# Optimization experiments

Hardware: AMD Instinct MI355X
Metric: run time of the kernel (lower is better)

Reference implementation:

```python
import jax, jax.numpy as jnp
import numpy as np

C = 256
R = 16
K = 7


def setup_inputs() -> dict:
    key = jax.random.key(0)
    k1, k2, k3, k4 = jax.random.split(key, 4)
    x = jax.random.normal(k1, (32, C, 64, 64), dtype=jnp.float32)
    # mlp: Conv2d(C, C//R, 1, bias=False) then Conv2d(C//R, C, 1, bias=False)
    w1 = jax.random.normal(k2, (C // R, C), dtype=jnp.float32) * (1.0 / np.sqrt(C))
    w2 = jax.random.normal(k3, (C, C // R), dtype=jnp.float32) * (1.0 / np.sqrt(C // R))
    # conv_spatial: Conv2d(2, 1, 7, padding=3, bias=False) -> OIHW [1,2,7,7]
    w_sp = jax.random.normal(k4, (1, 2, K, K), dtype=jnp.float32) * (1.0 / np.sqrt(2 * K * K))
    return {"x": x, "w1": w1, "w2": w2, "w_sp": w_sp}


def _cbam(x, w1, w2, w_sp):
    B, Cc, H, W = x.shape
    # --- channel attention ---
    avg = jnp.mean(x, axis=(2, 3))            # [B, C]
    mx = jnp.max(x, axis=(2, 3))              # [B, C]

    def mlp(v):
        h = jax.nn.relu(jnp.einsum('bc,rc->br', v, w1))  # [B, C//R]
        return jnp.einsum('br,cr->bc', h, w2)            # [B, C]

    ch_att = jax.nn.sigmoid(mlp(avg) + mlp(mx))          # [B, C]
    x = x * ch_att[:, :, None, None]

    # --- spatial attention ---
    avg_sp = jnp.mean(x, axis=1, keepdims=True)          # [B,1,H,W]
    max_sp = jnp.max(x, axis=1, keepdims=True)           # [B,1,H,W]
    sp = jnp.concatenate([avg_sp, max_sp], axis=1)       # [B,2,H,W]
    att = jax.lax.conv_general_dilated(
        sp, w_sp, window_strides=(1, 1), padding='SAME',
        dimension_numbers=('NCHW', 'OIHW', 'NCHW'))      # [B,1,H,W]
    return x * jax.nn.sigmoid(att)


def reference(x, w1, w2, w_sp):
    return _cbam(x, w1, w2, w_sp)
```

## Files before the change

kernel.cpp:

```cpp
#include <hip/hip_runtime.h>
#include <math.h>

#define Bn 32
#define Cn 256
#define Hn 64
#define Wn 64
#define HWn 4096
#define CRn 16

__device__ __forceinline__ float sigmoidf_(float v) { return 1.0f / (1.0f + __expf(-v)); }

__global__ __launch_bounds__(256) void k_chanstats(const float* __restrict__ x,
                                                   float* __restrict__ avg,
                                                   float* __restrict__ mx) {
    int bc = blockIdx.x;
    const float4* xv = (const float4*)(x + (size_t)bc * HWn);
    int t = threadIdx.x;
    float s = 0.0f, m = -INFINITY;
#pragma unroll
    for (int j = 0; j < 4; ++j) {
        float4 v = xv[t + j * 256];
        s += v.x + v.y + v.z + v.w;
        m = fmaxf(m, fmaxf(fmaxf(v.x, v.y), fmaxf(v.z, v.w)));
    }
#pragma unroll
    for (int off = 32; off > 0; off >>= 1) {
        s += __shfl_down(s, off);
        m = fmaxf(m, __shfl_down(m, off));
    }
    __shared__ float ss[4], sm[4];
    int wave = t >> 6, lane = t & 63;
    if (lane == 0) { ss[wave] = s; sm[wave] = m; }
    __syncthreads();
    if (t == 0) {
        s = ss[0] + ss[1] + ss[2] + ss[3];
        m = fmaxf(fmaxf(sm[0], sm[1]), fmaxf(sm[2], sm[3]));
        avg[bc] = s * (1.0f / HWn);
        mx[bc]  = m;
    }
}

__global__ __launch_bounds__(256) void k_mlp(const float* __restrict__ avg,
                                             const float* __restrict__ mx,
                                             const float* __restrict__ w1,
                                             const float* __restrict__ w2,
                                             float* __restrict__ ch_att) {
    int b = blockIdx.x;
    int t = threadIdx.x;
    __shared__ float sa[Cn], sx[Cn], h[2 * CRn];
    sa[t] = avg[b * Cn + t];
    sx[t] = mx[b * Cn + t];
    __syncthreads();
    if (t < 2 * CRn) {
        int r = t & (CRn - 1);
        const float* v = (t < CRn) ? sa : sx;
        float acc = 0.0f;
        for (int c = 0; c < Cn; ++c) acc += v[c] * w1[r * Cn + c];
        h[t] = fmaxf(acc, 0.0f);
    }
    __syncthreads();
    float acc = 0.0f;
#pragma unroll
    for (int r = 0; r < CRn; ++r) acc += (h[r] + h[CRn + r]) * w2[t * CRn + r];
    ch_att[b * Cn + t] = sigmoidf_(acc);
}

__global__ __launch_bounds__(256) void k_spstats(const float* __restrict__ x,
                                                 const float* __restrict__ ch_att,
                                                 float* __restrict__ avg_sp,
                                                 float* __restrict__ max_sp) {
    int blk = blockIdx.x;
    int b = blk >> 4;
    int hwbase = (blk & 15) * 256;
    int t = threadIdx.x;
    int tg = t >> 6;
    int lane = t & 63;

    __shared__ float satt[Cn];
    satt[t] = ch_att[b * Cn + t];
    __syncthreads();

    const float* xb = x + (size_t)b * Cn * HWn + hwbase;
    float4 s = {0.f, 0.f, 0.f, 0.f};
    float4 m = {-INFINITY, -INFINITY, -INFINITY, -INFINITY};
#pragma unroll 8
    for (int i = 0; i < 64; ++i) {
        int c = (tg << 6) + i;
        float4 v = ((const float4*)(xb + (size_t)c * HWn))[lane];
        float a = satt[c];
        v.x *= a; v.y *= a; v.z *= a; v.w *= a;
        s.x += v.x; s.y += v.y; s.z += v.z; s.w += v.w;
        m.x = fmaxf(m.x, v.x); m.y = fmaxf(m.y, v.y);
        m.z = fmaxf(m.z, v.z); m.w = fmaxf(m.w, v.w);
    }

    __shared__ float4 rs[4][64];
    __shared__ float4 rm[4][64];
    rs[tg][lane] = s;
    rm[tg][lane] = m;
    __syncthreads();
    if (tg == 0) {
#pragma unroll
        for (int g = 1; g < 4; ++g) {
            float4 os = rs[g][lane], om = rm[g][lane];
            s.x += os.x; s.y += os.y; s.z += os.z; s.w += os.w;
            m.x = fmaxf(m.x, om.x); m.y = fmaxf(m.y, om.y);
            m.z = fmaxf(m.z, om.z); m.w = fmaxf(m.w, om.w);
        }
        const float inv = 1.0f / Cn;
        float4 av = {s.x * inv, s.y * inv, s.z * inv, s.w * inv};
        ((float4*)(avg_sp + b * HWn + hwbase))[lane] = av;
        ((float4*)(max_sp + b * HWn + hwbase))[lane] = m;
    }
}

__global__ __launch_bounds__(256) void k_conv(const float* __restrict__ avg_sp,
                                              const float* __restrict__ max_sp,
                                              const float* __restrict__ w_sp,
                                              float* __restrict__ att) {
    int p = blockIdx.x * 256 + threadIdx.x;
    int b = p >> 12;
    int hw = p & (HWn - 1);
    int y = hw >> 6, xx = hw & 63;
    __shared__ float wk[98];
    if (threadIdx.x < 98) wk[threadIdx.x] = w_sp[threadIdx.x];
    __syncthreads();
    const float* ab = avg_sp + b * HWn;
    const float* mb = max_sp + b * HWn;
    float acc = 0.0f;
#pragma unroll
    for (int ky = 0; ky < 7; ++ky) {
        int yy = y + ky - 3;
        if (yy < 0 || yy >= Hn) continue;
#pragma unroll
        for (int kx = 0; kx < 7; ++kx) {
            int xc = xx + kx - 3;
            if (xc < 0 || xc >= Wn) continue;
            int q = yy * Wn + xc;
            acc += ab[q] * wk[ky * 7 + kx] + mb[q] * wk[49 + ky * 7 + kx];
        }
    }
    att[p] = sigmoidf_(acc);
}

__global__ __launch_bounds__(256) void k_final(const float* __restrict__ x,
                                               const float* __restrict__ ch_att,
                                               const float* __restrict__ att,
                                               float* __restrict__ out) {
    size_t f = (size_t)blockIdx.x * 256 + threadIdx.x;
    int bc  = (int)(f >> 10);
    int hw4 = (int)(f & 1023);
    int b = bc >> 8;
    float ca = ch_att[bc];
    float4 a = ((const float4*)(att + (size_t)b * HWn))[hw4];
    float4 v = ((const float4*)x)[f];
    float4 r;
    r.x = v.x * ca * a.x;
    r.y = v.y * ca * a.y;
    r.z = v.z * ca * a.z;
    r.w = v.w * ca * a.w;
    ((float4*)out)[f] = r;
}

extern "C" void kernel_launch(void* const* d_in, const int* in_sizes, int n_in,
                              void* d_out, int out_size, void* d_ws, size_t ws_size,
                              hipStream_t stream) {
    const float* x    = (const float*)d_in[0];
    const float* w1   = (const float*)d_in[1];
    const float* w2   = (const float*)d_in[2];
    const float* w_sp = (const float*)d_in[3];
    float* out = (float*)d_out;

    float* ws = (float*)d_ws;
    float* avg    = ws;
    float* mx     = avg + Bn * Cn;
    float* ch_att = mx + Bn * Cn;
    float* avg_sp = ch_att + Bn * Cn;
    float* max_sp = avg_sp + Bn * HWn;
    float* att    = max_sp + Bn * HWn;

    k_chanstats<<<Bn * Cn, 256, 0, stream>>>(x, avg, mx);
    k_mlp<<<Bn, 256, 0, stream>>>(avg, mx, w1, w2, ch_att);
    k_spstats<<<Bn * HWn / 256, 256, 0, stream>>>(x, ch_att, avg_sp, max_sp);
    k_conv<<<Bn * HWn / 256, 256, 0, stream>>>(avg_sp, max_sp, w_sp, att);
    k_final<<<(size_t)Bn * Cn * HWn / 4 / 256, 256, 0, stream>>>(x, ch_att, att, out);
}
```

Measured before the change: 286.1 us.

## Fuse spatial conv into final scaling kernel and retile spatial stats

Merges the 7x7 spatial conv with the final multiply. Each block loads a two-row halo of the pooled maps into shared memory, computes the sigmoid attention for two rows, then scales all channels for those rows, which removes one launch and the att buffer round trip. The spatial-stats kernel is retiled to 64-pixel segments with 16 channel groups and shuffle reductions, giving four times as many blocks. The channel MLP first layer is split across all 256 threads. Each fused block recomputes an 8-row halo, and per-row blocks issue smaller 256-byte contiguous accesses.

```diff
diff --git a/kernel.cpp b/kernel.cpp
--- a/kernel.cpp
+++ b/kernel.cpp
@@ -47,22 +47,33 @@
                                              float* __restrict__ ch_att) {
     int b = blockIdx.x;
     int t = threadIdx.x;
-    __shared__ float sa[Cn], sx[Cn], h[2 * CRn];
-    sa[t] = avg[b * Cn + t];
-    sx[t] = mx[b * Cn + t];
-    __syncthreads();
-    if (t < 2 * CRn) {
-        int r = t & (CRn - 1);
-        const float* v = (t < CRn) ? sa : sx;
-        float acc = 0.0f;
-        for (int c = 0; c < Cn; ++c) acc += v[c] * w1[r * Cn + c];
-        h[t] = fmaxf(acc, 0.0f);
-    }
-    __syncthreads();
+    __shared__ float sv[2][Cn];
+    __shared__ float part[32][8];
+    __shared__ float h[32];
+    sv[0][t] = avg[b * Cn + t];
+    sv[1][t] = mx[b * Cn + t];
+    __syncthreads();
+    int d  = t & 31;
+    int ch = t >> 5;
+    int r  = d & 15;
+    const float* v = sv[d >> 4];
+    const float* wrow = w1 + r * Cn + ch * 32;
     float acc = 0.0f;
 #pragma unroll
-    for (int r = 0; r < CRn; ++r) acc += (h[r] + h[CRn + r]) * w2[t * CRn + r];
-    ch_att[b * Cn + t] = sigmoidf_(acc);
+    for (int c = 0; c < 32; ++c) acc += v[ch * 32 + c] * wrow[c];
+    part[d][ch] = acc;
+    __syncthreads();
+    if (t < 32) {
+        float a = 0.0f;
+#pragma unroll
+        for (int k = 0; k < 8; ++k) a += part[t][k];
+        h[t] = fmaxf(a, 0.0f);
+    }
+    __syncthreads();
+    float acc2 = 0.0f;
+#pragma unroll
+    for (int rr = 0; rr < CRn; ++rr) acc2 += (h[rr] + h[CRn + rr]) * w2[t * CRn + rr];
+    ch_att[b * Cn + t] = sigmoidf_(acc2);
 }
 
 __global__ __launch_bounds__(256) void k_spstats(const float* __restrict__ x,
@@ -70,96 +81,129 @@
                                                  float* __restrict__ avg_sp,
                                                  float* __restrict__ max_sp) {
     int blk = blockIdx.x;
-    int b = blk >> 4;
-    int hwbase = (blk & 15) * 256;
-    int t = threadIdx.x;
-    int tg = t >> 6;
-    int lane = t & 63;
+    int b = blk >> 6;
+    int seg = blk & 63;
+    int t = threadIdx.x;
+    int f4 = t & 15;
+    int cg = t >> 4;
 
     __shared__ float satt[Cn];
     satt[t] = ch_att[b * Cn + t];
     __syncthreads();
 
-    const float* xb = x + (size_t)b * Cn * HWn + hwbase;
+    const float* xb = x + ((size_t)b * Cn) * HWn + seg * 64;
     float4 s = {0.f, 0.f, 0.f, 0.f};
     float4 m = {-INFINITY, -INFINITY, -INFINITY, -INFINITY};
-#pragma unroll 8
-    for (int i = 0; i < 64; ++i) {
-        int c = (tg << 6) + i;
-        float4 v = ((const float4*)(xb + (size_t)c * HWn))[lane];
+#pragma unroll
+    for (int i = 0; i < 16; ++i) {
+        int c = (i << 4) + cg;
+        float4 v = ((const float4*)(xb + (size_t)c * HWn))[f4];
         float a = satt[c];
         v.x *= a; v.y *= a; v.z *= a; v.w *= a;
         s.x += v.x; s.y += v.y; s.z += v.z; s.w += v.w;
         m.x = fmaxf(m.x, v.x); m.y = fmaxf(m.y, v.y);
         m.z = fmaxf(m.z, v.z); m.w = fmaxf(m.w, v.w);
     }
-
-    __shared__ float4 rs[4][64];
-    __shared__ float4 rm[4][64];
-    rs[tg][lane] = s;
-    rm[tg][lane] = m;
-    __syncthreads();
-    if (tg == 0) {
+#pragma unroll
+    for (int off = 32; off >= 16; off >>= 1) {
+        s.x += __shfl_down(s.x, off); s.y += __shfl_down(s.y, off);
+        s.z += __shfl_down(s.z, off); s.w += __shfl_down(s.w, off);
+        m.x = fmaxf(m.x, __shfl_down(m.x, off));
+        m.y = fmaxf(m.y, __shfl_down(m.y, off));
+        m.z = fmaxf(m.z, __shfl_down(m.z, off));
+        m.w = fmaxf(m.w, __shfl_down(m.w, off));
+    }
+    __shared__ float4 ps[4][16], pm[4][16];
+    int wave = t >> 6, lane = t & 63;
+    if (lane < 16) { ps[wave][lane] = s; pm[wave][lane] = m; }
+    __syncthreads();
+    if (t < 16) {
+        s = ps[0][t]; m = pm[0][t];
 #pragma unroll
         for (int g = 1; g < 4; ++g) {
-            float4 os = rs[g][lane], om = rm[g][lane];
+            float4 os = ps[g][t], om = pm[g][t];
             s.x += os.x; s.y += os.y; s.z += os.z; s.w += os.w;
             m.x = fmaxf(m.x, om.x); m.y = fmaxf(m.y, om.y);
             m.z = fmaxf(m.z, om.z); m.w = fmaxf(m.w, om.w);
         }
         const float inv = 1.0f / Cn;
         float4 av = {s.x * inv, s.y * inv, s.z * inv, s.w * inv};
-        ((float4*)(avg_sp + b * HWn + hwbase))[lane] = av;
-        ((float4*)(max_sp + b * HWn + hwbase))[lane] = m;
-    }
-}
-
-__global__ __launch_bounds__(256) void k_conv(const float* __restrict__ avg_sp,
-                                              const float* __restrict__ max_sp,
-                                              const float* __restrict__ w_sp,
-                                              float* __restrict__ att) {
-    int p = blockIdx.x * 256 + threadIdx.x;
-    int b = p >> 12;
-    int hw = p & (HWn - 1);
-    int y = hw >> 6, xx = hw & 63;
+        ((float4*)(avg_sp + b * HWn + seg * 64))[t] = av;
+        ((float4*)(max_sp + b * HWn + seg * 64))[t] = m;
+    }
+}
+
+__global__ __launch_bounds__(256) void k_convfinal(const float* __restrict__ x,
+                                                   const float* __restrict__ ch_att,
+                                                   const float* __restrict__ avg_sp,
+                                                   const float* __restrict__ max_sp,
+                                                   const float* __restrict__ w_sp,
+                                                   float* __restrict__ out) {
+    int blk = blockIdx.x;
+    int b = blk >> 5;
+    int y0 = (blk & 31) << 1;
+    int t = threadIdx.x;
+
+    __shared__ float ca[Cn];
     __shared__ float wk[98];
-    if (threadIdx.x < 98) wk[threadIdx.x] = w_sp[threadIdx.x];
-    __syncthreads();
+    __shared__ float ha[8][64];
+    __shared__ float hm[8][64];
+    __shared__ float att2[128];
+
+    ca[t] = ch_att[b * Cn + t];
+    if (t < 98) wk[t] = w_sp[t];
     const float* ab = avg_sp + b * HWn;
     const float* mb = max_sp + b * HWn;
-    float acc = 0.0f;
-#pragma unroll
-    for (int ky = 0; ky < 7; ++ky) {
-        int yy = y + ky - 3;
-        if (yy < 0 || yy >= Hn) continue;
-#pragma unroll
-        for (int kx = 0; kx < 7; ++kx) {
-            int xc = xx + kx - 3;
-            if (xc < 0 || xc >= Wn) continue;
-            int q = yy * Wn + xc;
-            acc += ab[q] * wk[ky * 7 + kx] + mb[q] * wk[49 + ky * 7 + kx];
+#pragma unroll
+    for (int k = 0; k < 4; ++k) {
+        int idx = k * 256 + t;
+        int mapi = idx >> 9;
+        int r = (idx >> 6) & 7;
+        int col = idx & 63;
+        int y = y0 - 3 + r;
+        float v = 0.0f;
+        if (y >= 0 && y < Hn) v = (mapi == 0 ? ab : mb)[y * Wn + col];
+        if (mapi == 0) ha[r][col] = v; else hm[r][col] = v;
+    }
+    __syncthreads();
+
+    if (t < 128) {
+        int row = t >> 6;
+        int col = t & 63;
+        float acc = 0.0f;
+#pragma unroll
+        for (int ky = 0; ky < 7; ++ky) {
+            int hr = row + ky;
+#pragma unroll
+            for (int kx = 0; kx < 7; ++kx) {
+                int xc = col + kx - 3;
+                if (xc < 0 || xc >= Wn) continue;
+                acc += ha[hr][xc] * wk[ky * 7 + kx] + hm[hr][xc] * wk[49 + ky * 7 + kx];
+            }
         }
-    }
-    att[p] = sigmoidf_(acc);
-}
-
-__global__ __launch_bounds__(256) void k_final(const float* __restrict__ x,
-                                               const float* __restrict__ ch_att,
-                                               const float* __restrict__ att,
-                                               float* __restrict__ out) {
-    size_t f = (size_t)blockIdx.x * 256 + threadIdx.x;
-    int bc  = (int)(f >> 10);
-    int hw4 = (int)(f & 1023);
-    int b = bc >> 8;
-    float ca = ch_att[bc];
-    float4 a = ((const float4*)(att + (size_t)b * HWn))[hw4];
-    float4 v = ((const float4*)x)[f];
-    float4 r;
-    r.x = v.x * ca * a.x;
-    r.y = v.y * ca * a.y;
-    r.z = v.z * ca * a.z;
-    r.w = v.w * ca * a.w;
-    ((float4*)out)[f] = r;
+        att2[t] = sigmoidf_(acc);
+    }
+    __syncthreads();
+
+    int f4 = t & 31;
+    int cg = t >> 5;
+    float4 a4 = ((const float4*)att2)[f4];
+    size_t base = ((size_t)b * Cn) * HWn + (size_t)y0 * Wn;
+    const float* xb = x + base;
+    float* ob = out + base;
+#pragma unroll 4
+    for (int i = 0; i < 32; ++i) {
+        int c = (i << 3) + cg;
+        size_t off = (size_t)c * HWn;
+        float4 v = ((const float4*)(xb + off))[f4];
+        float sfac = ca[c];
+        float4 rv;
+        rv.x = v.x * sfac * a4.x;
+        rv.y = v.y * sfac * a4.y;
+        rv.z = v.z * sfac * a4.z;
+        rv.w = v.w * sfac * a4.w;
+        ((float4*)(ob + off))[f4] = rv;
+    }
 }
 
 extern "C" void kernel_launch(void* const* d_in, const int* in_sizes, int n_in,
@@ -177,11 +221,9 @@
     float* ch_att = mx + Bn * Cn;
     float* avg_sp = ch_att + Bn * Cn;
     float* max_sp = avg_sp + Bn * HWn;
-    float* att    = max_sp + Bn * HWn;
 
     k_chanstats<<<Bn * Cn, 256, 0, stream>>>(x, avg, mx);
     k_mlp<<<Bn, 256, 0, stream>>>(avg, mx, w1, w2, ch_att);
-    k_spstats<<<Bn * HWn / 256, 256, 0, stream>>>(x, ch_att, avg_sp, max_sp);
-    k_conv<<<Bn * HWn / 256, 256, 0, stream>>>(avg_sp, max_sp, w_sp, att);
-    k_final<<<(size_t)Bn * Cn * HWn / 4 / 256, 256, 0, stream>>>(x, ch_att, att, out);
-}
+    k_spstats<<<Bn * 64, 256, 0, stream>>>(x, ch_att, avg_sp, max_sp);
+    k_convfinal<<<Bn * 32, 256, 0, stream>>>(x, ch_att, avg_sp, max_sp, w_sp, out);
+}
```

Measured after the change: 289.4 us. No clear change (+1.2%).
